# Performance work log

Hardware: AMD Instinct MI355X
Metric: run time of the kernel (lower is better)

The kernel has to match this reference:

```python
import jax, jax.numpy as jnp
import numpy as np
from jax import lax

DEPTH = 3  # signature truncation depth
B, L, I, H, O = 256, 512, 32, 16, 10
SIG_DIM = H + H**2 + H**3  # 4368 = signatory.signature_channels(16, 3)


def setup_inputs() -> dict:
    key = jax.random.key(0)
    ks = jax.random.split(key, 7)
    s = 1.0 / np.sqrt(H).astype(np.float32)
    sf = 1.0 / np.sqrt(SIG_DIM).astype(np.float32)
    return {
        "X": jax.random.normal(ks[0], (B, L, I), jnp.float32),
        "W_ih": jax.random.uniform(ks[1], (4 * H, I), jnp.float32, -s, s),
        "W_hh": jax.random.uniform(ks[2], (4 * H, H), jnp.float32, -s, s),
        "b_ih": jax.random.uniform(ks[3], (4 * H,), jnp.float32, -s, s),
        "b_hh": jax.random.uniform(ks[4], (4 * H,), jnp.float32, -s, s),
        "fc_w": jax.random.uniform(ks[5], (O, SIG_DIM), jnp.float32, -sf, sf),
        "fc_b": jax.random.uniform(ks[6], (O,), jnp.float32, -sf, sf),
    }


def _lstm(X, W_ih, W_hh, b_ih, b_hh):
    # torch nn.LSTM, single layer, batch_first, gate order (i, f, g, o)
    b, l, _ = X.shape
    h0 = jnp.zeros((b, H), X.dtype)
    c0 = jnp.zeros((b, H), X.dtype)
    # precompute input projection for all timesteps: [L, B, 4H]
    xw = jnp.swapaxes(jnp.einsum('bli,gi->blg', X, W_ih) + b_ih + b_hh, 0, 1)

    def step(carry, xw_t):
        h, c = carry
        gates = xw_t + h @ W_hh.T
        i, f, g, o = jnp.split(gates, 4, axis=-1)
        c = jax.nn.sigmoid(f) * c + jax.nn.sigmoid(i) * jnp.tanh(g)
        h = jax.nn.sigmoid(o) * jnp.tanh(c)
        return (h, c), h

    _, hs = lax.scan(step, (h0, c0), xw)  # hs: [L, B, H]
    return jnp.swapaxes(hs, 0, 1)  # [B, L, H]


def _outer(a, b):
    # batched flattened tensor product: [B, m] x [B, n] -> [B, m*n]
    return (a[:, :, None] * b[:, None, :]).reshape(a.shape[0], -1)


def _signature(h, depth):
    # signatory.signature: Chen's identity scan over path increments,
    # returns concatenated levels 1..depth: [B, C + C^2 + ... + C^depth]
    b, l, c = h.shape
    dx = jnp.swapaxes(h[:, 1:] - h[:, :-1], 0, 1)  # [L-1, B, C]
    S0 = tuple(jnp.zeros((b, c ** (k + 1)), h.dtype) for k in range(depth))

    def step(S, d):
        # exp(d) levels: e_k = d^{tensor k} / k!
        e = [d]
        for k in range(2, depth + 1):
            e.append(_outer(e[-1], d) / k)
        # S <- S (x) exp(d), truncated:  newS_k = S_k + sum_{j=1..k-1} S_{k-j} (x) e_j + e_k
        newS = []
        for k in range(1, depth + 1):
            acc = S[k - 1] + e[k - 1]
            for j in range(1, k):
                acc = acc + _outer(S[k - j - 1], e[j - 1])
            newS.append(acc)
        return tuple(newS), None

    S, _ = lax.scan(step, S0, dx)
    return jnp.concatenate(S, axis=-1)  # [B, SIG_DIM]


def reference(X, W_ih, W_hh, b_ih, b_hh, fc_w, fc_b):
    hseq = _lstm(X, W_ih, W_hh, b_ih, b_hh)           # [B, L, H]
    sig = _signature(hseq, DEPTH)                      # [B, SIG_DIM]
    out = sig @ fc_w.T + fc_b                          # [B, O]
    return out.reshape(-1, O)
```

## Files before the change

kernel.cpp:

```cpp
#include <hip/hip_runtime.h>

#define NB 256
#define NL 512
#define NI 32
#define NH 16
#define NG 64
#define SIGD 4368
#define XS 516

__device__ __forceinline__ float RL(float v, int lane) {
  return __builtin_bit_cast(float, __builtin_amdgcn_readlane(__builtin_bit_cast(int, v), lane));
}
template<int CTRL>
__device__ __forceinline__ float QB(float v) {
  return __builtin_bit_cast(float, __builtin_amdgcn_update_dpp(
      0, __builtin_bit_cast(int, v), CTRL, 0xF, 0xF, true));
}
__device__ __forceinline__ int cutf(int k) {
  switch (k) {
    case 1: return 24;  case 2: return 102; case 3: return 180; case 4: return 258;
    case 5: return 335; case 6: return 412; case 7: return 488; case 8: return 511;
    default: return 0;
  }
}

__global__ __launch_bounds__(512, 1) void k_main(const float* __restrict__ X,
    const float* __restrict__ Wih, const float* __restrict__ bih,
    const float* __restrict__ bhh, const float* __restrict__ Whh,
    const float* __restrict__ fcw, const float* __restrict__ fcb,
    float* __restrict__ out) {
  __shared__ __align__(16) float xwT[NG * XS];
  __shared__ __align__(16) float bnd[144];
  __shared__ int prog;
  int tid = threadIdx.x;
  int wv = tid >> 6;
  int ln = tid & 63;
  int b = blockIdx.x;

  if (tid == 0) prog = -1;

  {
    const float Kg = (ln >= 32 && ln < 48) ? 2.885390082f : -1.442695041f;
    float w2[NI];
#pragma unroll
    for (int i = 0; i < 8; ++i) {
      float4 v = *(const float4*)(Wih + ln * NI + 4 * i);
      w2[4*i+0] = v.x; w2[4*i+1] = v.y; w2[4*i+2] = v.z; w2[4*i+3] = v.w;
    }
    float bias = bih[ln] + bhh[ln];
    const float* xb = X + (size_t)b * NL * NI;
#pragma unroll 4
    for (int t = 64 * wv; t < 64 * (wv + 1); ++t) {
      const float4* xr = (const float4*)(xb + t * NI);
      float x0 = bias, x1 = 0.f, x2 = 0.f, x3 = 0.f;
#pragma unroll
      for (int i = 0; i < 8; ++i) {
        float4 xv = xr[i];
        x0 += xv.x * w2[4*i+0]; x1 += xv.y * w2[4*i+1];
        x2 += xv.z * w2[4*i+2]; x3 += xv.w * w2[4*i+3];
      }
      xwT[ln * XS + t] = Kg * ((x0 + x1) + (x2 + x3));
    }
  }
  __syncthreads();

  if (wv == 0) {
    __asm__ __volatile__("s_setprio 3");
    const int q = ln & 3;
    const int j = ln >> 2;
    const int gmem = q * 16 + j;
    const bool isg = (q == 2);
    const float Kg = isg ? 2.885390082f : -1.442695041f;
    const float CT = 2.885390082f;
    const float Av = isg ? -2.0f : (q == 0 ? CT : 1.0f);
    const float Bv = isg ? 1.0f : 0.0f;
    float w[NH];
#pragma unroll
    for (int qq = 0; qq < 4; ++qq) {
      float4 v = *(const float4*)(Whh + gmem * NH + 4 * qq);
      w[4*qq+0] = Kg*v.x; w[4*qq+1] = Kg*v.y; w[4*qq+2] = Kg*v.z; w[4*qq+3] = Kg*v.w;
    }
    const float* xt = xwT + gmem * XS;
    float* hdst = xwT + j * XS + 4 * q;
    float4 xq[4];
#pragma unroll
    for (int i = 0; i < 4; ++i) xq[i] = *(const float4*)(xt + 4 * i);
    float cs = 0.0f, hval = 0.0f;
    float hst[4] = {0.f, 0.f, 0.f, 0.f};
    for (int tb = 0; tb < NL; tb += 16) {
#pragma unroll
      for (int k = 0; k < 16; ++k) {
        int t = tb + k;
        float hs[16];
#pragma unroll
        for (int u = 0; u < 16; ++u) hs[u] = RL(hval, 4 * u);
        float xval = ((const float*)xq)[k];
        if ((k & 3) == 3 && t + 16 < NL)
          xq[k >> 2] = *(const float4*)(xt + (t + 13));
        float a0 = xval, a1 = 0.f, a2 = 0.f, a3 = 0.f;
        float a4 = 0.f,  a5 = 0.f, a6 = 0.f, a7 = 0.f;
#pragma unroll
        for (int u = 0; u < 2; ++u) {
          a0 += hs[8*u+0] * w[8*u+0];
          a1 += hs[8*u+1] * w[8*u+1];
          a2 += hs[8*u+2] * w[8*u+2];
          a3 += hs[8*u+3] * w[8*u+3];
          a4 += hs[8*u+4] * w[8*u+4];
          a5 += hs[8*u+5] * w[8*u+5];
          a6 += hs[8*u+6] * w[8*u+6];
          a7 += hs[8*u+7] * w[8*u+7];
        }
        float acc = ((a0 + a1) + (a2 + a3)) + ((a4 + a5) + (a6 + a7));
        float e = __builtin_amdgcn_exp2f(acc);
        float r = __builtin_amdgcn_rcpf(1.0f + e);
        float val = __builtin_fmaf(Av, r, Bv);
        float iv = QB<0x00>(val);
        float fv = QB<0x55>(val);
        float gv = QB<0xAA>(val);
        float ov = QB<0xFF>(val);
        cs = __builtin_fmaf(fv, cs, iv * gv);
        float e2 = __builtin_amdgcn_exp2f(cs);
        float tc = __builtin_fmaf(-2.0f, __builtin_amdgcn_rcpf(1.0f + e2), 1.0f);
        hval = ov * tc;
        hst[k & 3] = (q == (k >> 2)) ? hval : hst[k & 3];
      }
      float4 hv;
      hv.x = hst[0]; hv.y = hst[1]; hv.z = hst[2]; hv.w = hst[3];
      *(float4*)(hdst + tb) = hv;
      __asm__ __volatile__("" ::: "memory");
      if (ln == 0) *(volatile int*)&prog = tb + 15;
    }
    __asm__ __volatile__("s_setprio 0");
  }

  int ch = wv;
  if (wv == 0) ch = 7;
  else if (wv == 4) ch = 0;
  else if (wv == 7) ch = 4;
  const int bi = ln & 15;
  const int hi = ln >> 4;
  int ts = cutf(ch);
  int te = cutf(ch + 1);
  while (*(volatile int*)&prog < te) __builtin_amdgcn_s_sleep(8);
  __asm__ __volatile__("" ::: "memory");

  float s3[4][16];
  float s2[4] = {0.f, 0.f, 0.f, 0.f};
#pragma unroll
  for (int m = 0; m < 4; ++m)
#pragma unroll
    for (int cc = 0; cc < 16; ++cc) s3[m][cc] = 0.f;

  float hA[16], hB[16];
  float hAb, hBb;
  float hAa[4], hBa[4], h0a[4];
#pragma unroll
  for (int cc = 0; cc < 16; ++cc) hA[cc] = xwT[cc * XS + ts];
  hAb = xwT[bi * XS + ts];
#pragma unroll
  for (int m = 0; m < 4; ++m) { hAa[m] = xwT[(4 * m + hi) * XS + ts]; h0a[m] = hAa[m]; }

  auto SSTEP = [&](float (&hc16)[16], float& hcb, float (&hca)[4],
                   float (&hn16)[16], float& hnb, float (&hna)[4], int tn) {
#pragma unroll
    for (int cc = 0; cc < 16; ++cc) hn16[cc] = xwT[cc * XS + tn];
    hnb = xwT[bi * XS + tn];
    float d[16];
#pragma unroll
    for (int cc = 0; cc < 16; ++cc) d[cc] = hn16[cc] - hc16[cc];
    float db = hnb - hcb;
    float P[4];
#pragma unroll
    for (int m = 0; m < 4; ++m) {
      hna[m] = xwT[(4 * m + hi) * XS + tn];
      float da = hna[m] - hca[m];
      float s1 = hca[m] - h0a[m];
      P[m] = s2[m] + db * (0.5f * s1 + 0.166666666667f * da);
      s2[m] += db * (s1 + 0.5f * da);
    }
#pragma unroll
    for (int m = 0; m < 4; ++m)
#pragma unroll
      for (int cc = 0; cc < 16; ++cc)
        s3[m][cc] += P[m] * d[cc];
  };

  {
    int t = ts;
    for (; t + 2 <= te; t += 2) {
      SSTEP(hA, hAb, hAa, hB, hBb, hBa, t + 1);
      SSTEP(hB, hBb, hBa, hA, hAb, hAa, t + 2);
    }
    if (t < te) SSTEP(hA, hAb, hAa, hB, hBb, hBa, t + 1);
  }
  __syncthreads();

  if (tid < 144) {
    int k = tid >> 4, j = tid & 15;
    bnd[tid] = xwT[j * XS + cutf(k)];
  }
  __syncthreads();

  float* slot0 = xwT;
  float* slot1 = xwT + 4352;
  float* sigb  = xwT + 8704;
  auto writeSlot = [&](float* slot) {
#pragma unroll
    for (int m = 0; m < 4; ++m) slot[64 * m + ln] = s2[m];
    float* s3s = slot + 256;
#pragma unroll
    for (int m = 0; m < 4; ++m)
#pragma unroll
      for (int cc = 0; cc < 16; ++cc)
        s3s[64 * ln + ((m * 16 + cc) ^ (ln & 31))] = s3[m][cc];
  };
  auto combineSlot = [&](const float* slot, int as_, int ae_, int bs_, int be_) {
    const float* s2b = slot;
    const float* s3b = slot + 256;
    float s1b[16];
#pragma unroll
    for (int cc = 0; cc < 16; ++cc) s1b[cc] = bnd[be_ * 16 + cc] - bnd[bs_ * 16 + cc];
    float s1bb = bnd[be_ * 16 + bi] - bnd[bs_ * 16 + bi];
    float s1aa[4];
#pragma unroll
    for (int m = 0; m < 4; ++m) {
      int a = 4 * m + hi;
      s1aa[m] = bnd[ae_ * 16 + a] - bnd[as_ * 16 + a];
    }
    float row[16];
#pragma unroll
    for (int cc = 0; cc < 16; ++cc) row[cc] = s2b[bi * 16 + cc];
#pragma unroll
    for (int m = 0; m < 4; ++m) {
      float s2bo = s2b[64 * m + ln];
#pragma unroll
      for (int cc = 0; cc < 16; ++cc)
        s3[m][cc] += s3b[64 * ln + ((m * 16 + cc) ^ (ln & 31))]
                   + s2[m] * s1b[cc] + s1aa[m] * row[cc];
      s2[m] += s2bo + s1aa[m] * s1bb;
    }
  };
  if (ch == 1) writeSlot(slot0);
  if (ch == 3) writeSlot(slot1);
  __syncthreads();
  if (ch == 0) combineSlot(slot0, 0, 1, 1, 2);
  if (ch == 2) combineSlot(slot1, 2, 3, 3, 4);
  __syncthreads();
  if (ch == 5) writeSlot(slot0);
  if (ch == 7) writeSlot(slot1);
  __syncthreads();
  if (ch == 4) combineSlot(slot0, 4, 5, 5, 6);
  if (ch == 6) combineSlot(slot1, 6, 7, 7, 8);
  __syncthreads();
  if (ch == 2) writeSlot(slot0);
  if (ch == 6) writeSlot(slot1);
  __syncthreads();
  if (ch == 0) combineSlot(slot0, 0, 2, 2, 4);
  if (ch == 4) combineSlot(slot1, 4, 6, 6, 8);
  __syncthreads();
  if (ch == 4) writeSlot(slot0);
  __syncthreads();
  if (ch == 0) {
    combineSlot(slot0, 0, 4, 4, 8);
    if (ln < 16) sigb[ln] = bnd[8 * 16 + ln] - bnd[ln];
#pragma unroll
    for (int m = 0; m < 4; ++m) sigb[16 + 64 * m + ln] = s2[m];
#pragma unroll
    for (int m = 0; m < 4; ++m) {
#pragma unroll
      for (int qq = 0; qq < 4; ++qq) {
        float4 v;
        v.x = s3[m][4*qq+0]; v.y = s3[m][4*qq+1]; v.z = s3[m][4*qq+2]; v.w = s3[m][4*qq+3];
        *(float4*)(sigb + 272 + 1024 * m + 256 * hi + 16 * bi + 4 * qq) = v;
      }
    }
  }
  __syncthreads();

  {
    float acc[10];
#pragma unroll
    for (int o = 0; o < 10; ++o) acc[o] = 0.f;
    for (int k = tid; k < SIGD; k += 512) {
      float s = sigb[k];
#pragma unroll
      for (int o = 0; o < 10; ++o) acc[o] += s * fcw[o * SIGD + k];
    }
#pragma unroll
    for (int o = 0; o < 10; ++o) {
      float v = acc[o];
#pragma unroll
      for (int off = 32; off > 0; off >>= 1) v += __shfl_down(v, off);
      if (ln == 0) bnd[wv * 10 + o] = v;
    }
    __syncthreads();
    if (tid < 10) {
      float s = fcb[tid];
#pragma unroll
      for (int w = 0; w < 8; ++w) s += bnd[w * 10 + tid];
      out[b * 10 + tid] = s;
    }
  }
}

extern "C" void kernel_launch(void* const* d_in, const int* in_sizes, int n_in,
                              void* d_out, int out_size, void* d_ws, size_t ws_size,
                              hipStream_t stream) {
  const float* X   = (const float*)d_in[0];
  const float* Wih = (const float*)d_in[1];
  const float* Whh = (const float*)d_in[2];
  const float* bih = (const float*)d_in[3];
  const float* bhh = (const float*)d_in[4];
  const float* fcw = (const float*)d_in[5];
  const float* fcb = (const float*)d_in[6];
  float* out = (float*)d_out;
  k_main<<<NB, 512, 0, stream>>>(X, Wih, bih, bhh, Whh, fcw, fcb, out);
}
```

Baseline: 196.4 us.

## Stream signature accumulation in one wave concurrently with LSTM recurrence

Replaces the eight-wave chunked signature computation and its tree of Chen-identity merges with a single wave (wave 1) that consumes hidden states as the LSTM wave publishes them, polling the progress counter. This overlaps the signature scan with the serial recurrence and removes the merge stages, their barriers and the boundary buffer. The cost is that the signature work is now serial over all 511 steps in one wave, so the kernel only benefits if that wave keeps pace with the LSTM. Other waves sit idle until the final FC reduction.

```diff
diff --git a/kernel.cpp b/kernel.cpp
--- a/kernel.cpp
+++ b/kernel.cpp
@@ -16,13 +16,6 @@
   return __builtin_bit_cast(float, __builtin_amdgcn_update_dpp(
       0, __builtin_bit_cast(int, v), CTRL, 0xF, 0xF, true));
 }
-__device__ __forceinline__ int cutf(int k) {
-  switch (k) {
-    case 1: return 24;  case 2: return 102; case 3: return 180; case 4: return 258;
-    case 5: return 335; case 6: return 412; case 7: return 488; case 8: return 511;
-    default: return 0;
-  }
-}
 
 __global__ __launch_bounds__(512, 1) void k_main(const float* __restrict__ X,
     const float* __restrict__ Wih, const float* __restrict__ bih,
@@ -30,7 +23,7 @@
     const float* __restrict__ fcw, const float* __restrict__ fcb,
     float* __restrict__ out) {
   __shared__ __align__(16) float xwT[NG * XS];
-  __shared__ __align__(16) float bnd[144];
+  __shared__ __align__(16) float red[80];
   __shared__ int prog;
   int tid = threadIdx.x;
   int wv = tid >> 6;
@@ -131,138 +124,69 @@
       if (ln == 0) *(volatile int*)&prog = tb + 15;
     }
     __asm__ __volatile__("s_setprio 0");
-  }
-
-  int ch = wv;
-  if (wv == 0) ch = 7;
-  else if (wv == 4) ch = 0;
-  else if (wv == 7) ch = 4;
-  const int bi = ln & 15;
-  const int hi = ln >> 4;
-  int ts = cutf(ch);
-  int te = cutf(ch + 1);
-  while (*(volatile int*)&prog < te) __builtin_amdgcn_s_sleep(8);
-  __asm__ __volatile__("" ::: "memory");
-
-  float s3[4][16];
-  float s2[4] = {0.f, 0.f, 0.f, 0.f};
-#pragma unroll
-  for (int m = 0; m < 4; ++m)
-#pragma unroll
-    for (int cc = 0; cc < 16; ++cc) s3[m][cc] = 0.f;
-
-  float hA[16], hB[16];
-  float hAb, hBb;
-  float hAa[4], hBa[4], h0a[4];
-#pragma unroll
-  for (int cc = 0; cc < 16; ++cc) hA[cc] = xwT[cc * XS + ts];
-  hAb = xwT[bi * XS + ts];
-#pragma unroll
-  for (int m = 0; m < 4; ++m) { hAa[m] = xwT[(4 * m + hi) * XS + ts]; h0a[m] = hAa[m]; }
-
-  auto SSTEP = [&](float (&hc16)[16], float& hcb, float (&hca)[4],
-                   float (&hn16)[16], float& hnb, float (&hna)[4], int tn) {
-#pragma unroll
-    for (int cc = 0; cc < 16; ++cc) hn16[cc] = xwT[cc * XS + tn];
-    hnb = xwT[bi * XS + tn];
-    float d[16];
-#pragma unroll
-    for (int cc = 0; cc < 16; ++cc) d[cc] = hn16[cc] - hc16[cc];
-    float db = hnb - hcb;
-    float P[4];
-#pragma unroll
-    for (int m = 0; m < 4; ++m) {
-      hna[m] = xwT[(4 * m + hi) * XS + tn];
-      float da = hna[m] - hca[m];
-      float s1 = hca[m] - h0a[m];
-      P[m] = s2[m] + db * (0.5f * s1 + 0.166666666667f * da);
-      s2[m] += db * (s1 + 0.5f * da);
-    }
+  } else if (wv == 1) {
+    const int bi = ln & 15;
+    const int hi = ln >> 4;
+    float s3[4][16];
+    float s2[4] = {0.f, 0.f, 0.f, 0.f};
 #pragma unroll
     for (int m = 0; m < 4; ++m)
 #pragma unroll
-      for (int cc = 0; cc < 16; ++cc)
-        s3[m][cc] += P[m] * d[cc];
-  };
-
-  {
-    int t = ts;
-    for (; t + 2 <= te; t += 2) {
-      SSTEP(hA, hAb, hAa, hB, hBb, hBa, t + 1);
-      SSTEP(hB, hBb, hBa, hA, hAb, hAa, t + 2);
-    }
-    if (t < te) SSTEP(hA, hAb, hAa, hB, hBb, hBa, t + 1);
-  }
-  __syncthreads();
-
-  if (tid < 144) {
-    int k = tid >> 4, j = tid & 15;
-    bnd[tid] = xwT[j * XS + cutf(k)];
-  }
-  __syncthreads();
-
-  float* slot0 = xwT;
-  float* slot1 = xwT + 4352;
-  float* sigb  = xwT + 8704;
-  auto writeSlot = [&](float* slot) {
-#pragma unroll
-    for (int m = 0; m < 4; ++m) slot[64 * m + ln] = s2[m];
-    float* s3s = slot + 256;
-#pragma unroll
-    for (int m = 0; m < 4; ++m)
-#pragma unroll
-      for (int cc = 0; cc < 16; ++cc)
-        s3s[64 * ln + ((m * 16 + cc) ^ (ln & 31))] = s3[m][cc];
-  };
-  auto combineSlot = [&](const float* slot, int as_, int ae_, int bs_, int be_) {
-    const float* s2b = slot;
-    const float* s3b = slot + 256;
-    float s1b[16];
-#pragma unroll
-    for (int cc = 0; cc < 16; ++cc) s1b[cc] = bnd[be_ * 16 + cc] - bnd[bs_ * 16 + cc];
-    float s1bb = bnd[be_ * 16 + bi] - bnd[bs_ * 16 + bi];
-    float s1aa[4];
-#pragma unroll
-    for (int m = 0; m < 4; ++m) {
-      int a = 4 * m + hi;
-      s1aa[m] = bnd[ae_ * 16 + a] - bnd[as_ * 16 + a];
-    }
-    float row[16];
-#pragma unroll
-    for (int cc = 0; cc < 16; ++cc) row[cc] = s2b[bi * 16 + cc];
-#pragma unroll
-    for (int m = 0; m < 4; ++m) {
-      float s2bo = s2b[64 * m + ln];
-#pragma unroll
-      for (int cc = 0; cc < 16; ++cc)
-        s3[m][cc] += s3b[64 * ln + ((m * 16 + cc) ^ (ln & 31))]
-                   + s2[m] * s1b[cc] + s1aa[m] * row[cc];
-      s2[m] += s2bo + s1aa[m] * s1bb;
-    }
-  };
-  if (ch == 1) writeSlot(slot0);
-  if (ch == 3) writeSlot(slot1);
-  __syncthreads();
-  if (ch == 0) combineSlot(slot0, 0, 1, 1, 2);
-  if (ch == 2) combineSlot(slot1, 2, 3, 3, 4);
-  __syncthreads();
-  if (ch == 5) writeSlot(slot0);
-  if (ch == 7) writeSlot(slot1);
-  __syncthreads();
-  if (ch == 4) combineSlot(slot0, 4, 5, 5, 6);
-  if (ch == 6) combineSlot(slot1, 6, 7, 7, 8);
-  __syncthreads();
-  if (ch == 2) writeSlot(slot0);
-  if (ch == 6) writeSlot(slot1);
-  __syncthreads();
-  if (ch == 0) combineSlot(slot0, 0, 2, 2, 4);
-  if (ch == 4) combineSlot(slot1, 4, 6, 6, 8);
-  __syncthreads();
-  if (ch == 4) writeSlot(slot0);
-  __syncthreads();
-  if (ch == 0) {
-    combineSlot(slot0, 0, 4, 4, 8);
-    if (ln < 16) sigb[ln] = bnd[8 * 16 + ln] - bnd[ln];
+      for (int cc = 0; cc < 16; ++cc) s3[m][cc] = 0.f;
+
+    int avail;
+    while ((avail = *(volatile int*)&prog) < 15) __builtin_amdgcn_s_sleep(2);
+    __asm__ __volatile__("" ::: "memory");
+
+    float hA[16], hB[16];
+    float hAb, hBb;
+    float hAa[4], hBa[4], h0a[4];
+#pragma unroll
+    for (int cc = 0; cc < 16; ++cc) hA[cc] = xwT[cc * XS + 0];
+    hAb = xwT[bi * XS + 0];
+#pragma unroll
+    for (int m = 0; m < 4; ++m) { hAa[m] = xwT[(4 * m + hi) * XS + 0]; h0a[m] = hAa[m]; }
+
+    auto SSTEP = [&](float (&hc16)[16], float& hcb, float (&hca)[4],
+                     float (&hn16)[16], float& hnb, float (&hna)[4], int tn) {
+#pragma unroll
+      for (int cc = 0; cc < 16; ++cc) hn16[cc] = xwT[cc * XS + tn];
+      hnb = xwT[bi * XS + tn];
+      float d[16];
+#pragma unroll
+      for (int cc = 0; cc < 16; ++cc) d[cc] = hn16[cc] - hc16[cc];
+      float db = hnb - hcb;
+      float P[4];
+#pragma unroll
+      for (int m = 0; m < 4; ++m) {
+        hna[m] = xwT[(4 * m + hi) * XS + tn];
+        float da = hna[m] - hca[m];
+        float s1 = hca[m] - h0a[m];
+        P[m] = s2[m] + db * (0.5f * s1 + 0.166666666667f * da);
+        s2[m] += db * (s1 + 0.5f * da);
+      }
+#pragma unroll
+      for (int m = 0; m < 4; ++m)
+#pragma unroll
+        for (int cc = 0; cc < 16; ++cc)
+          s3[m][cc] += P[m] * d[cc];
+    };
+
+    for (int p = 0; p < 255; ++p) {
+      int tn2 = 2 * p + 2;
+      if (tn2 > avail) {
+        while ((avail = *(volatile int*)&prog) < tn2) __builtin_amdgcn_s_sleep(2);
+        __asm__ __volatile__("" ::: "memory");
+      }
+      SSTEP(hA, hAb, hAa, hB, hBb, hBa, 2 * p + 1);
+      SSTEP(hB, hBb, hBa, hA, hAb, hAa, 2 * p + 2);
+    }
+    while ((avail = *(volatile int*)&prog) < 511) __builtin_amdgcn_s_sleep(2);
+    __asm__ __volatile__("" ::: "memory");
+    SSTEP(hA, hAb, hAa, hB, hBb, hBa, 511);
+
+    float* sigb = xwT + 16 * XS;
+    if (ln < 16) sigb[ln] = xwT[ln * XS + 511] - xwT[ln * XS + 0];
 #pragma unroll
     for (int m = 0; m < 4; ++m) sigb[16 + 64 * m + ln] = s2[m];
 #pragma unroll
@@ -278,6 +202,7 @@
   __syncthreads();
 
   {
+    const float* sigb = xwT + 16 * XS;
     float acc[10];
 #pragma unroll
     for (int o = 0; o < 10; ++o) acc[o] = 0.f;
@@ -291,13 +216,13 @@
       float v = acc[o];
 #pragma unroll
       for (int off = 32; off > 0; off >>= 1) v += __shfl_down(v, off);
-      if (ln == 0) bnd[wv * 10 + o] = v;
+      if (ln == 0) red[wv * 10 + o] = v;
     }
     __syncthreads();
     if (tid < 10) {
       float s = fcb[tid];
 #pragma unroll
-      for (int w = 0; w < 8; ++w) s += bnd[w * 10 + tid];
+      for (int w = 0; w < 8; ++w) s += red[w * 10 + tid];
       out[b * 10 + tid] = s;
     }
   }
```

New measurement: 265.2 us. 35.0% more time.
